# Optimization experiments

Hardware: AMD Instinct MI355X
Metric: run time of the kernel (lower is better)

## Reference

```python
import jax, jax.numpy as jnp
import numpy as np

V, H, NH, L, NL = 30522, 768, 12, 4, 2  # vocab, hidden, heads, layers, labels
B, S = 4, 1024
HD = H // NH  # head dim = 64


def setup_inputs() -> dict:
    key = jax.random.key(0)
    ks = jax.random.split(key, 16)
    sc = 0.02
    return {
        "input_ids": jax.random.randint(ks[0], (B, S), 0, V),
        "emb": jax.random.normal(ks[1], (V, H), jnp.float32) * sc,
        "Wq": jax.random.normal(ks[2], (L, H, H), jnp.float32) * sc,
        "bq": jnp.zeros((L, H), jnp.float32),
        "Wk": jax.random.normal(ks[3], (L, H, H), jnp.float32) * sc,
        "bk": jnp.zeros((L, H), jnp.float32),
        "Wv": jax.random.normal(ks[4], (L, H, H), jnp.float32) * sc,
        "bv": jnp.zeros((L, H), jnp.float32),
        "Wi": jax.random.normal(ks[5], (L, H, H), jnp.float32) * sc,
        "bi": jnp.zeros((L, H), jnp.float32),
        "Wo": jax.random.normal(ks[6], (L, H, H), jnp.float32) * sc,
        "bo": jnp.zeros((L, H), jnp.float32),
        "Wc": jax.random.normal(ks[7], (NL, H), jnp.float32) * sc,
        "bc": jnp.zeros((NL,), jnp.float32),
    }


def _encoder(x, Wq, bq, Wk, bk, Wv, bv, Wi, bi, Wo, bo):
    def layer(h, p):
        wq, bq_, wk, bk_, wv, bv_, wi, bi_, wo, bo_ = p
        def heads(y):  # [B,S,H] -> [B,NH,S,HD]
            return y.reshape(B, S, NH, HD).transpose(0, 2, 1, 3)
        q = heads(h @ wq.T + bq_)
        k = heads(h @ wk.T + bk_)
        v = heads(h @ wv.T + bv_)
        scores = jnp.einsum("bhqd,bhkd->bhqk", q, k) / jnp.sqrt(jnp.float32(HD))
        probs = jax.nn.softmax(scores, axis=-1)  # dropout is identity (eval)
        ctx = jnp.einsum("bhqk,bhkd->bhqd", probs, v)
        attn_out = ctx.transpose(0, 2, 1, 3).reshape(B, S, H)
        inter = jax.nn.relu(attn_out @ wi.T + bi_)
        out = inter @ wo.T + bo_ + attn_out  # residual adds attention output
        return out, None

    x, _ = jax.lax.scan(layer, x, (Wq, bq, Wk, bk, Wv, bv, Wi, bi, Wo, bo))
    return x


def reference(input_ids, emb, Wq, bq, Wk, bk, Wv, bv, Wi, bi, Wo, bo, Wc, bc):
    x = emb[input_ids]  # [B,S,H]
    x = _encoder(x, Wq, bq, Wk, bk, Wv, bv, Wi, bi, Wo, bo)
    pooled = x[:, 0]  # [B,H]
    logits = pooled @ Wc.T + bc  # [B,NL]
    return logits
```

## Files before the change

### kernel.cpp

```cpp
#include <hip/hip_runtime.h>
#include <hip/hip_bf16.h>
#include <math.h>

constexpr int Hdim = 768;
constexpr int NH   = 12;
constexpr int HD   = 64;
constexpr int NLAYER = 4;
constexpr int Bb   = 4;
constexpr int Ss   = 1024;
constexpr int Mm   = Bb * Ss;
constexpr int NL   = 2;
constexpr int PL   = Bb * NH * Ss;
constexpr float LOG2E = 1.44269504088896f;

typedef _Float16 f16x8 __attribute__((ext_vector_type(8)));
typedef _Float16 f16x4 __attribute__((ext_vector_type(4)));
typedef __fp16   h16x2 __attribute__((ext_vector_type(2)));
typedef float    f32x4 __attribute__((ext_vector_type(4)));

__device__ __forceinline__ f32x4 mfma32h(f16x8 a, f16x8 b, f32x4 c) {
#if __has_builtin(__builtin_amdgcn_mfma_f32_16x16x32_f16)
    return __builtin_amdgcn_mfma_f32_16x16x32_f16(a, b, c, 0, 0, 0);
#else
    asm("v_mfma_f32_16x16x32_f16 %0, %1, %2, %0" : "+v"(c) : "v"(a), "v"(b));
    return c;
#endif
}
__device__ __forceinline__ f32x4 mfma16h(f16x4 a, f16x4 b, f32x4 c) {
#if __has_builtin(__builtin_amdgcn_mfma_f32_16x16x16f16)
    return __builtin_amdgcn_mfma_f32_16x16x16f16(a, b, c, 0, 0, 0);
#else
    asm("v_mfma_f32_16x16x16_f16 %0, %1, %2, %0" : "+v"(c) : "v"(a), "v"(b));
    return c;
#endif
}

__device__ __forceinline__ void gload16(const void* g, void* l) {
    __builtin_amdgcn_global_load_lds(
        (const __attribute__((address_space(1))) unsigned int*)g,
        (__attribute__((address_space(3))) unsigned int*)l, 16, 0, 0);
}

__global__ void embed_kernel(const int* __restrict__ ids,
                             const float* __restrict__ emb,
                             float* __restrict__ x32, _Float16* __restrict__ xh) {
    int row = blockIdx.x;
    int t = threadIdx.x;
    int id = ids[row];
    float4 v = ((const float4*)(emb + (size_t)id * Hdim))[t];
    ((float4*)(x32 + (size_t)row * Hdim))[t] = v;
    f16x4 h;
    h[0] = (_Float16)v.x; h[1] = (_Float16)v.y;
    h[2] = (_Float16)v.z; h[3] = (_Float16)v.w;
    *(f16x4*)(xh + (size_t)row * Hdim + t * 4) = h;
}

__global__ void cvtw_kernel(const float* __restrict__ Wq, const float* __restrict__ Wk,
                            const float* __restrict__ Wv, const float* __restrict__ Wi,
                            const float* __restrict__ Wo,
                            _Float16* __restrict__ out) {
    int i = blockIdx.x * 256 + threadIdx.x;
    int l = i / (5 * 147456);
    int rem = i - l * (5 * 147456);
    int which = rem / 147456;
    int j = rem - which * 147456;
    const float* src = (which == 0 ? Wq : which == 1 ? Wk : which == 2 ? Wv
                      : which == 3 ? Wi : Wo) + (size_t)l * 589824;
    float4 v = ((const float4*)src)[j];
    f16x4 h;
    h[0] = (_Float16)v.x; h[1] = (_Float16)v.y;
    h[2] = (_Float16)v.z; h[3] = (_Float16)v.w;
    *(f16x4*)(out + ((size_t)l * 5 + which) * 589824 + (size_t)j * 4) = h;
}

__global__ __launch_bounds__(256) void gemm_f16(
    const _Float16* __restrict__ Xh, const _Float16* __restrict__ Wh,
    const float* __restrict__ b0, const float* __restrict__ b1,
    const float* __restrict__ b2,
    const float* __restrict__ resid32,
    _Float16* __restrict__ Yh, float* __restrict__ Y32,
    int relu, size_t outSeg, float qscale, int gm)
{
    __shared__ _Float16 lds[12288];

    const int tid = threadIdx.x;
    const int lane = tid & 63, w = tid >> 6;
    const int l15 = lane & 15, g = lane >> 4;
    const int wr = w >> 1, wc = w & 1;

    const int nwg = gridDim.x;
    const int cpx = nwg >> 3;
    const int bid = blockIdx.x;
    const int x   = (bid & 7) * cpx + (bid >> 3);
    const int m0  = (x % gm) * 64;
    const int n0  = (x / gm) * 128;

    const int srow = lane >> 3;
    const int sswz = 8 * ((lane & 7) ^ srow);
    const _Float16* pA = Xh + (size_t)(m0 + w*16 + srow) * Hdim + sswz;
    const _Float16* pB = Wh + (size_t)(n0 + w*32 + srow) * Hdim + sswz;
    _Float16* lA = &lds[0]    + w * 1024;
    _Float16* lB = &lds[4096] + w * 2048;

    f32x4 acc[2][4];
    #pragma unroll
    for (int m = 0; m < 2; ++m)
        #pragma unroll
        for (int n = 0; n < 4; ++n) acc[m][n] = (f32x4){0.f, 0.f, 0.f, 0.f};

    const int fsw = l15 & 7;

    for (int k0 = 0; k0 < Hdim; k0 += 64) {
        __syncthreads();
        gload16(pA + k0,          lA);
        gload16(pA + k0 + 8*Hdim, lA + 512);
        #pragma unroll
        for (int j = 0; j < 4; ++j)
            gload16(pB + k0 + j*8*Hdim, lB + j*512);
        __syncthreads();

        #pragma unroll
        for (int ks = 0; ks < 2; ++ks) {
            const int so = 8 * ((ks*4 + g) ^ fsw);
            f16x8 af[2], bf[4];
            #pragma unroll
            for (int m = 0; m < 2; ++m)
                af[m] = *(const f16x8*)&lds[(wr*32 + m*16 + l15) * 64 + so];
            #pragma unroll
            for (int n = 0; n < 4; ++n)
                bf[n] = *(const f16x8*)&lds[4096 + (wc*64 + n*16 + l15) * 64 + so];
            #pragma unroll
            for (int m = 0; m < 2; ++m)
                #pragma unroll
                for (int n = 0; n < 4; ++n)
                    acc[m][n] = mfma32h(af[m], bf[n], acc[m][n]);
        }
    }

    const int rb = m0 + wr*32 + g*4;
    #pragma unroll
    for (int n = 0; n < 4; ++n) {
        const int col = n0 + wc*64 + n*16 + l15;
        const int seg = col / Hdim;
        const int lc  = col - seg * Hdim;
        const float bias = (seg == 0 ? b0 : seg == 1 ? b1 : b2)[lc];
        #pragma unroll
        for (int m = 0; m < 2; ++m) {
            #pragma unroll
            for (int r = 0; r < 4; ++r) {
                const size_t idx = (size_t)seg * outSeg + (size_t)(rb + m*16 + r) * Hdim + lc;
                float v = acc[m][n][r] + bias;
                if (seg == 0) v *= qscale;
                if (relu) v = v > 0.f ? v : 0.f;
                if (resid32) v += resid32[idx];
                Yh[idx] = (_Float16)v;
                if (Y32) Y32[idx] = v;
            }
        }
    }
}

__global__ __launch_bounds__(256, 3) void attn_mfma(
    const _Float16* __restrict__ Qh, const _Float16* __restrict__ Kh,
    const _Float16* __restrict__ Vh,
    float* __restrict__ Op0, float* __restrict__ Op1,
    float* __restrict__ Mp, float* __restrict__ Lp)
{
    __shared__ _Float16 sm[17408];

    const int tid  = threadIdx.x;
    const int lane = tid & 63, wid = tid >> 6;
    const int l15  = lane & 15, g = lane >> 4;
    const int qtile = blockIdx.x >> 1, part = blockIdx.x & 1;
    const int h = blockIdx.y, b = blockIdx.z;

    const size_t rowbase = (size_t)b * Ss;
    const int    colbase = h * HD;
    const int    q0 = qtile * 128 + wid * 32;
    const int    kv0 = part * 512;

    f16x8 qf[2][2];
    #pragma unroll
    for (int nf = 0; nf < 2; ++nf) {
        const size_t r = (rowbase + q0 + nf * 16 + l15) * Hdim + colbase;
        #pragma unroll
        for (int ks = 0; ks < 2; ++ks)
            qf[nf][ks] = *(const f16x8*)(Qh + r + ks * 32 + g * 8);
    }

    f32x4 accO[4][2];
    #pragma unroll
    for (int mf = 0; mf < 4; ++mf)
        #pragma unroll
        for (int nf = 0; nf < 2; ++nf) accO[mf][nf] = (f32x4){0.f, 0.f, 0.f, 0.f};
    float mrun[2] = {-1e30f, -1e30f}, lsum[2] = {0.f, 0.f};

    const int s8 = lane >> 3;
    const int kswz = 8 * ((lane & 7) ^ s8);
    const _Float16* gK = Kh + (rowbase + kv0 + wid*16 + s8) * Hdim + colbase + kswz;

    const int kx = lane ^ (wid << 4);
    const _Float16* gV = Vh + (rowbase + kv0 + lane) * Hdim + colbase + wid * 16;
    uint4 vr[2];

    const int fsw = l15 & 7;

    gload16(gK,          &sm[0] + wid*1024);
    gload16(gK + 8*Hdim, &sm[0] + wid*1024 + 512);
    #pragma unroll
    for (int u = 0; u < 2; ++u) vr[u] = *(const uint4*)(gV + u * 8);
    #pragma unroll
    for (int u = 0; u < 2; ++u) {
        const _Float16* hs = (const _Float16*)&vr[u];
        #pragma unroll
        for (int j = 0; j < 8; ++j)
            sm[8192 + (wid*16 + u*8 + j) * 72 + kx] = hs[j];
    }
    __syncthreads();

    for (int t = 0; t < 8; ++t) {
        const int cur = t & 1;
        const int kb = cur * 4096;
        const int vb = 8192 + cur * 4608;
        if (t < 7) {
            const int nkb = (cur ^ 1) * 4096;
            const size_t ko = (size_t)((t + 1) * 64) * Hdim;
            gload16(gK + ko,          &sm[nkb] + wid*1024);
            gload16(gK + ko + 8*Hdim, &sm[nkb] + wid*1024 + 512);
            #pragma unroll
            for (int u = 0; u < 2; ++u)
                vr[u] = *(const uint4*)(gV + ko + u * 8);
        }

        f32x4 sc[4][2];
        #pragma unroll
        for (int m = 0; m < 4; ++m)
            #pragma unroll
            for (int nf = 0; nf < 2; ++nf) sc[m][nf] = (f32x4){0.f, 0.f, 0.f, 0.f};
        __builtin_amdgcn_s_setprio(1);
        #pragma unroll
        for (int ks = 0; ks < 2; ++ks) {
            const int so = 8 * ((ks*4 + g) ^ fsw);
            #pragma unroll
            for (int m = 0; m < 4; ++m) {
                f16x8 kh_ = *(const f16x8*)&sm[kb + (m * 16 + l15) * 64 + so];
                #pragma unroll
                for (int nf = 0; nf < 2; ++nf)
                    sc[m][nf] = mfma32h(kh_, qf[nf][ks], sc[m][nf]);
            }
        }
        __builtin_amdgcn_s_setprio(0);

        f16x4 pb[4][2];
        #pragma unroll
        for (int nf = 0; nf < 2; ++nf) {
            float tl = -1e30f;
            #pragma unroll
            for (int m = 0; m < 4; ++m)
                #pragma unroll
                for (int r = 0; r < 4; ++r) tl = fmaxf(tl, sc[m][nf][r]);
            if (__any(tl > mrun[nf] + 11.5416f)) {
                float tmax = fmaxf(tl, __shfl_xor(tl, 16));
                tmax = fmaxf(tmax, __shfl_xor(tmax, 32));
                const float mnew = fmaxf(mrun[nf], tmax);
                const float corr = __builtin_amdgcn_exp2f(mrun[nf] - mnew);
                mrun[nf] = mnew;
                lsum[nf] *= corr;
                #pragma unroll
                for (int mf = 0; mf < 4; ++mf) {
                    accO[mf][nf][0] *= corr; accO[mf][nf][1] *= corr;
                    accO[mf][nf][2] *= corr; accO[mf][nf][3] *= corr;
                }
            }
            float ps = 0.f;
            #pragma unroll
            for (int m = 0; m < 4; ++m)
                #pragma unroll
                for (int r = 0; r < 4; ++r) {
                    const float p = __builtin_amdgcn_exp2f(sc[m][nf][r] - mrun[nf]);
                    sc[m][nf][r] = p;
                    ps += p;
                }
            lsum[nf] += ps;
            #pragma unroll
            for (int kt = 0; kt < 4; ++kt) {
                union { h16x2 h2[2]; f16x4 v; } u;
                u.h2[0] = __builtin_amdgcn_cvt_pkrtz(sc[kt][nf][0], sc[kt][nf][1]);
                u.h2[1] = __builtin_amdgcn_cvt_pkrtz(sc[kt][nf][2], sc[kt][nf][3]);
                pb[kt][nf] = u.v;
            }
        }

        if (t < 7) {
            const int nvb = 8192 + (cur ^ 1) * 4608;
            #pragma unroll
            for (int u = 0; u < 2; ++u) {
                const _Float16* hs = (const _Float16*)&vr[u];
                #pragma unroll
                for (int j = 0; j < 8; ++j)
                    sm[nvb + (wid*16 + u*8 + j) * 72 + kx] = hs[j];
            }
        }

        __builtin_amdgcn_s_setprio(1);
        #pragma unroll
        for (int kt = 0; kt < 4; ++kt)
            #pragma unroll
            for (int mf = 0; mf < 4; ++mf) {
                const int voff = vb + (mf * 16 + l15) * 72 + ((kt ^ mf) * 16 + g * 4);
                f16x4 vh_ = *(const f16x4*)&sm[voff];
                #pragma unroll
                for (int nf = 0; nf < 2; ++nf)
                    accO[mf][nf] = mfma16h(vh_, pb[kt][nf], accO[mf][nf]);
            }
        __builtin_amdgcn_s_setprio(0);

        __syncthreads();
    }

    #pragma unroll
    for (int nf = 0; nf < 2; ++nf) {
        lsum[nf] += __shfl_xor(lsum[nf], 16);
        lsum[nf] += __shfl_xor(lsum[nf], 32);
    }
    float* ot = (float*)sm + wid * 2176;
    #pragma unroll
    for (int nf = 0; nf < 2; ++nf) {
        #pragma unroll
        for (int mf = 0; mf < 4; ++mf)
            #pragma unroll
            for (int r = 0; r < 4; ++r)
                ot[(nf * 16 + l15) * 68 + mf * 16 + g * 4 + r] = accO[mf][nf][r];
    }
    if (g == 0) {
        #pragma unroll
        for (int nf = 0; nf < 2; ++nf) {
            const size_t idx = (size_t)part * PL +
                (((size_t)b * NH + h) * Ss + q0 + nf * 16 + l15);
            Mp[idx] = mrun[nf];
            Lp[idx] = lsum[nf];
        }
    }
    __syncthreads();
    float* Op = part ? Op1 : Op0;
    const int orow = lane >> 1, oc = (lane & 1) * 32;
    const size_t pbase = (((size_t)b * NH + h) * Ss + q0 + orow) * 64 + oc;
    #pragma unroll
    for (int i = 0; i < 8; ++i)
        *(float4*)(Op + pbase + i * 4) = *(float4*)&ot[orow * 68 + oc + i * 4];
}

__global__ void merge_kernel(const float* __restrict__ Op0, const float* __restrict__ Op1,
                             const float* __restrict__ Mp, const float* __restrict__ Lp,
                             _Float16* __restrict__ a16, float* __restrict__ a32) {
    const int id = blockIdx.x * 256 + threadIdx.x;
    const int idx = id >> 2, dseg = id & 3;
    const int b = idx / (NH * Ss);
    const int rem = idx - b * NH * Ss;
    const int h = rem / Ss, q = rem - h * Ss;
    const float m0 = Mp[idx], m1 = Mp[PL + idx];
    const float l0 = Lp[idx], l1 = Lp[PL + idx];
    const float M  = fmaxf(m0, m1);
    const float e0 = __builtin_amdgcn_exp2f(m0 - M);
    const float e1 = __builtin_amdgcn_exp2f(m1 - M);
    const float inv = 1.f / (l0 * e0 + l1 * e1);
    const size_t pb = (size_t)idx * 64 + dseg * 16;
    const size_t ga = ((size_t)(b * Ss + q)) * Hdim + h * 64 + dseg * 16;
    #pragma unroll
    for (int i = 0; i < 4; ++i) {
        float4 a = *(const float4*)(Op0 + pb + i * 4);
        float4 c = *(const float4*)(Op1 + pb + i * 4);
        float4 o;
        o.x = (a.x * e0 + c.x * e1) * inv;
        o.y = (a.y * e0 + c.y * e1) * inv;
        o.z = (a.z * e0 + c.z * e1) * inv;
        o.w = (a.w * e0 + c.w * e1) * inv;
        *(float4*)(a32 + ga + i * 4) = o;
        f16x4 hh;
        hh[0] = (_Float16)o.x; hh[1] = (_Float16)o.y;
        hh[2] = (_Float16)o.z; hh[3] = (_Float16)o.w;
        *(f16x4*)(a16 + ga + i * 4) = hh;
    }
}

__global__ void cls_kernel(const float* __restrict__ x32,
                           const float* __restrict__ Wc,
                           const float* __restrict__ bc,
                           float* __restrict__ out) {
    const int b = blockIdx.x >> 1;
    const int n = blockIdx.x & 1;
    const int t = threadIdx.x;
    const float* px = x32 + (size_t)b * Ss * Hdim;
    const float* pw = Wc + (size_t)n * Hdim;
    float partial = 0.f;
    for (int k = t; k < Hdim; k += 256) partial = fmaf(px[k], pw[k], partial);
    __shared__ float red[256];
    red[t] = partial;
    __syncthreads();
    for (int off = 128; off > 0; off >>= 1) {
        if (t < off) red[t] += red[t + off];
        __syncthreads();
    }
    if (t == 0) out[blockIdx.x] = red[0] + bc[n];
}

extern "C" void kernel_launch(void* const* d_in, const int* in_sizes, int n_in,
                              void* d_out, int out_size, void* d_ws, size_t ws_size,
                              hipStream_t stream) {
    const int*   ids = (const int*)d_in[0];
    const float* emb = (const float*)d_in[1];
    const float* Wq  = (const float*)d_in[2];
    const float* bq  = (const float*)d_in[3];
    const float* Wk  = (const float*)d_in[4];
    const float* bk  = (const float*)d_in[5];
    const float* Wv  = (const float*)d_in[6];
    const float* bv  = (const float*)d_in[7];
    const float* Wi  = (const float*)d_in[8];
    const float* bi  = (const float*)d_in[9];
    const float* Wo  = (const float*)d_in[10];
    const float* bo  = (const float*)d_in[11];
    const float* Wc  = (const float*)d_in[12];
    const float* bc  = (const float*)d_in[13];
    float* out = (float*)d_out;

    const size_t F  = (size_t)Mm * Hdim;
    const size_t WS = (size_t)Hdim * Hdim;

    float*    x32 = (float*)d_ws;
    _Float16* xh  = (_Float16*)(x32 + F);
    _Float16* qkv = xh + F;
    _Float16* a16 = qkv + 3 * F;
    _Float16* i16 = a16 + F;
    _Float16* w16 = i16 + F;
    float*    a32 = (float*)(w16 + 20 * WS);
    float*    Op0 = a32 + F;
    float*    Op1 = Op0 + F;
    float*    Mp  = Op1 + F;
    float*    Lp  = Mp + 2 * PL;

    embed_kernel<<<Mm, 192, 0, stream>>>(ids, emb, x32, xh);
    cvtw_kernel<<<NLAYER * 5 * 147456 / 256, 256, 0, stream>>>(Wq, Wk, Wv, Wi, Wo, w16);

    for (int l = 0; l < NLAYER; ++l) {
        _Float16* wl = w16 + (size_t)l * 5 * WS;
        gemm_f16<<<1152, 256, 0, stream>>>(
            xh, wl, bq + l*Hdim, bk + l*Hdim, bv + l*Hdim,
            nullptr, qkv, nullptr, 0, F, 0.125f * LOG2E, 64);
        attn_mfma<<<dim3(16, NH, Bb), 256, 0, stream>>>(
            qkv, qkv + F, qkv + 2*F, Op0, Op1, Mp, Lp);
        merge_kernel<<<PL * 4 / 256, 256, 0, stream>>>(Op0, Op1, Mp, Lp, a16, a32);
        gemm_f16<<<384, 256, 0, stream>>>(
            a16, wl + 3*WS, bi + l*Hdim, bi + l*Hdim, bi + l*Hdim,
            nullptr, i16, nullptr, 1, 0, 1.f, 64);
        gemm_f16<<<384, 256, 0, stream>>>(
            i16, wl + 4*WS, bo + l*Hdim, bo + l*Hdim, bo + l*Hdim,
            a32, xh, x32, 0, 0, 1.f, 64);
    }

    cls_kernel<<<Bb * NL, 256, 0, stream>>>(x32, Wc, bc, out);
}
```

Measured before the change: 436.6 us.

## Add 32-row GEMM tile for small GEMMs, merge prep kernels, raise attention occupancy

Templates the GEMM on its M tile size. A 32-row variant launches 768 blocks instead of 384 for the two 768-wide GEMMs, so more of the GPU's compute units have work. The embedding and weight-conversion kernels are merged into one launch, and the attention kernel's launch bounds now request 4 waves per SIMD instead of 3. The smaller tiles reduce data reuse per block, and the higher occupancy target may force register spills.

Result: faster. 412.6 us (-5.5%).

```diff
diff --git a/kernel.cpp b/kernel.cpp
--- a/kernel.cpp
+++ b/kernel.cpp
@@ -41,38 +41,40 @@
         (__attribute__((address_space(3))) unsigned int*)l, 16, 0, 0);
 }
 
-__global__ void embed_kernel(const int* __restrict__ ids,
-                             const float* __restrict__ emb,
-                             float* __restrict__ x32, _Float16* __restrict__ xh) {
-    int row = blockIdx.x;
-    int t = threadIdx.x;
-    int id = ids[row];
-    float4 v = ((const float4*)(emb + (size_t)id * Hdim))[t];
-    ((float4*)(x32 + (size_t)row * Hdim))[t] = v;
-    f16x4 h;
-    h[0] = (_Float16)v.x; h[1] = (_Float16)v.y;
-    h[2] = (_Float16)v.z; h[3] = (_Float16)v.w;
-    *(f16x4*)(xh + (size_t)row * Hdim + t * 4) = h;
-}
-
-__global__ void cvtw_kernel(const float* __restrict__ Wq, const float* __restrict__ Wk,
+__global__ void prep_kernel(const int* __restrict__ ids,
+                            const float* __restrict__ emb,
+                            float* __restrict__ x32, _Float16* __restrict__ xh,
+                            const float* __restrict__ Wq, const float* __restrict__ Wk,
                             const float* __restrict__ Wv, const float* __restrict__ Wi,
                             const float* __restrict__ Wo,
-                            _Float16* __restrict__ out) {
-    int i = blockIdx.x * 256 + threadIdx.x;
-    int l = i / (5 * 147456);
-    int rem = i - l * (5 * 147456);
-    int which = rem / 147456;
-    int j = rem - which * 147456;
-    const float* src = (which == 0 ? Wq : which == 1 ? Wk : which == 2 ? Wv
-                      : which == 3 ? Wi : Wo) + (size_t)l * 589824;
-    float4 v = ((const float4*)src)[j];
-    f16x4 h;
-    h[0] = (_Float16)v.x; h[1] = (_Float16)v.y;
-    h[2] = (_Float16)v.z; h[3] = (_Float16)v.w;
-    *(f16x4*)(out + ((size_t)l * 5 + which) * 589824 + (size_t)j * 4) = h;
-}
-
+                            _Float16* __restrict__ w16) {
+    if (blockIdx.x < 3072) {
+        int gidx = blockIdx.x * 256 + threadIdx.x;
+        int row = gidx / 192, t = gidx - row * 192;
+        int id = ids[row];
+        float4 v = ((const float4*)(emb + (size_t)id * Hdim))[t];
+        ((float4*)(x32 + (size_t)row * Hdim))[t] = v;
+        f16x4 h;
+        h[0] = (_Float16)v.x; h[1] = (_Float16)v.y;
+        h[2] = (_Float16)v.z; h[3] = (_Float16)v.w;
+        *(f16x4*)(xh + (size_t)row * Hdim + t * 4) = h;
+    } else {
+        int i = (blockIdx.x - 3072) * 256 + threadIdx.x;
+        int l = i / (5 * 147456);
+        int rem = i - l * (5 * 147456);
+        int which = rem / 147456;
+        int j = rem - which * 147456;
+        const float* src = (which == 0 ? Wq : which == 1 ? Wk : which == 2 ? Wv
+                          : which == 3 ? Wi : Wo) + (size_t)l * 589824;
+        float4 v = ((const float4*)src)[j];
+        f16x4 h;
+        h[0] = (_Float16)v.x; h[1] = (_Float16)v.y;
+        h[2] = (_Float16)v.z; h[3] = (_Float16)v.w;
+        *(f16x4*)(w16 + ((size_t)l * 5 + which) * 589824 + (size_t)j * 4) = h;
+    }
+}
+
+template<int BM>
 __global__ __launch_bounds__(256) void gemm_f16(
     const _Float16* __restrict__ Xh, const _Float16* __restrict__ Wh,
     const float* __restrict__ b0, const float* __restrict__ b1,
@@ -81,39 +83,51 @@
     _Float16* __restrict__ Yh, float* __restrict__ Y32,
     int relu, size_t outSeg, float qscale, int gm)
 {
-    __shared__ _Float16 lds[12288];
+    constexpr int ABASE = BM * 64;
+    constexpr int NFR   = (BM == 64) ? 4 : 2;
+    __shared__ _Float16 lds[ABASE + 8192];
 
     const int tid = threadIdx.x;
     const int lane = tid & 63, w = tid >> 6;
     const int l15 = lane & 15, g = lane >> 4;
-    const int wr = w >> 1, wc = w & 1;
 
     const int nwg = gridDim.x;
     const int cpx = nwg >> 3;
     const int bid = blockIdx.x;
     const int x   = (bid & 7) * cpx + (bid >> 3);
-    const int m0  = (x % gm) * 64;
+    const int m0  = (x % gm) * BM;
     const int n0  = (x / gm) * 128;
 
     const int srow = lane >> 3;
     const int sswz = 8 * ((lane & 7) ^ srow);
-    const _Float16* pA = Xh + (size_t)(m0 + w*16 + srow) * Hdim + sswz;
+    const _Float16* pA;
+    _Float16* lA;
+    if constexpr (BM == 64) {
+        pA = Xh + (size_t)(m0 + w*16 + srow) * Hdim + sswz;
+        lA = &lds[0] + w * 1024;
+    } else {
+        pA = Xh + (size_t)(m0 + w*8 + srow) * Hdim + sswz;
+        lA = &lds[0] + w * 512;
+    }
     const _Float16* pB = Wh + (size_t)(n0 + w*32 + srow) * Hdim + sswz;
-    _Float16* lA = &lds[0]    + w * 1024;
-    _Float16* lB = &lds[4096] + w * 2048;
-
-    f32x4 acc[2][4];
+    _Float16* lB = &lds[ABASE] + w * 2048;
+
+    f32x4 acc[2][NFR];
     #pragma unroll
     for (int m = 0; m < 2; ++m)
         #pragma unroll
-        for (int n = 0; n < 4; ++n) acc[m][n] = (f32x4){0.f, 0.f, 0.f, 0.f};
+        for (int n = 0; n < NFR; ++n) acc[m][n] = (f32x4){0.f, 0.f, 0.f, 0.f};
 
     const int fsw = l15 & 7;
 
     for (int k0 = 0; k0 < Hdim; k0 += 64) {
         __syncthreads();
-        gload16(pA + k0,          lA);
-        gload16(pA + k0 + 8*Hdim, lA + 512);
+        if constexpr (BM == 64) {
+            gload16(pA + k0,          lA);
+            gload16(pA + k0 + 8*Hdim, lA + 512);
+        } else {
+            gload16(pA + k0, lA);
+        }
         #pragma unroll
         for (int j = 0; j < 4; ++j)
             gload16(pB + k0 + j*8*Hdim, lB + j*512);
@@ -122,25 +136,32 @@
         #pragma unroll
         for (int ks = 0; ks < 2; ++ks) {
             const int so = 8 * ((ks*4 + g) ^ fsw);
-            f16x8 af[2], bf[4];
+            f16x8 af[2], bf[NFR];
+            #pragma unroll
+            for (int m = 0; m < 2; ++m) {
+                const int ar = (BM == 64) ? ((w >> 1)*32 + m*16 + l15)
+                                          : (m*16 + l15);
+                af[m] = *(const f16x8*)&lds[ar * 64 + so];
+            }
+            #pragma unroll
+            for (int n = 0; n < NFR; ++n) {
+                const int br = (BM == 64) ? ((w & 1)*64 + n*16 + l15)
+                                          : (w*32 + n*16 + l15);
+                bf[n] = *(const f16x8*)&lds[ABASE + br * 64 + so];
+            }
             #pragma unroll
             for (int m = 0; m < 2; ++m)
-                af[m] = *(const f16x8*)&lds[(wr*32 + m*16 + l15) * 64 + so];
-            #pragma unroll
-            for (int n = 0; n < 4; ++n)
-                bf[n] = *(const f16x8*)&lds[4096 + (wc*64 + n*16 + l15) * 64 + so];
-            #pragma unroll
-            for (int m = 0; m < 2; ++m)
-                #pragma unroll
-                for (int n = 0; n < 4; ++n)
+                #pragma unroll
+                for (int n = 0; n < NFR; ++n)
                     acc[m][n] = mfma32h(af[m], bf[n], acc[m][n]);
         }
     }
 
-    const int rb = m0 + wr*32 + g*4;
-    #pragma unroll
-    for (int n = 0; n < 4; ++n) {
-        const int col = n0 + wc*64 + n*16 + l15;
+    const int rb = (BM == 64) ? (m0 + (w >> 1)*32 + g*4) : (m0 + g*4);
+    #pragma unroll
+    for (int n = 0; n < NFR; ++n) {
+        const int col = (BM == 64) ? (n0 + (w & 1)*64 + n*16 + l15)
+                                   : (n0 + w*32 + n*16 + l15);
         const int seg = col / Hdim;
         const int lc  = col - seg * Hdim;
         const float bias = (seg == 0 ? b0 : seg == 1 ? b1 : b2)[lc];
@@ -160,7 +181,7 @@
     }
 }
 
-__global__ __launch_bounds__(256, 3) void attn_mfma(
+__global__ __launch_bounds__(256, 4) void attn_mfma(
     const _Float16* __restrict__ Qh, const _Float16* __restrict__ Kh,
     const _Float16* __restrict__ Vh,
     float* __restrict__ Op0, float* __restrict__ Op1,
@@ -438,23 +459,22 @@
     float*    Mp  = Op1 + F;
     float*    Lp  = Mp + 2 * PL;
 
-    embed_kernel<<<Mm, 192, 0, stream>>>(ids, emb, x32, xh);
-    cvtw_kernel<<<NLAYER * 5 * 147456 / 256, 256, 0, stream>>>(Wq, Wk, Wv, Wi, Wo, w16);
+    prep_kernel<<<14592, 256, 0, stream>>>(ids, emb, x32, xh, Wq, Wk, Wv, Wi, Wo, w16);
 
     for (int l = 0; l < NLAYER; ++l) {
         _Float16* wl = w16 + (size_t)l * 5 * WS;
-        gemm_f16<<<1152, 256, 0, stream>>>(
+        gemm_f16<64><<<1152, 256, 0, stream>>>(
             xh, wl, bq + l*Hdim, bk + l*Hdim, bv + l*Hdim,
             nullptr, qkv, nullptr, 0, F, 0.125f * LOG2E, 64);
         attn_mfma<<<dim3(16, NH, Bb), 256, 0, stream>>>(
             qkv, qkv + F, qkv + 2*F, Op0, Op1, Mp, Lp);
         merge_kernel<<<PL * 4 / 256, 256, 0, stream>>>(Op0, Op1, Mp, Lp, a16, a32);
-        gemm_f16<<<384, 256, 0, stream>>>(
+        gemm_f16<32><<<768, 256, 0, stream>>>(
             a16, wl + 3*WS, bi + l*Hdim, bi + l*Hdim, bi + l*Hdim,
-            nullptr, i16, nullptr, 1, 0, 1.f, 64);
-        gemm_f16<<<384, 256, 0, stream>>>(
+            nullptr, i16, nullptr, 1, 0, 1.f, 128);
+        gemm_f16<32><<<768, 256, 0, stream>>>(
             i16, wl + 4*WS, bo + l*Hdim, bo + l*Hdim, bo + l*Hdim,
-            a32, xh, x32, 0, 0, 1.f, 64);
+            a32, xh, x32, 0, 0, 1.f, 128);
     }
 
     cls_kernel<<<Bb * NL, 256, 0, stream>>>(x32, Wc, bc, out);
```
